# Kernel tuning notes

Measured on AMD Instinct MI355X. Metric: run time of the kernel, lower is better.

The kernel has to match this reference:

```python
import jax, jax.numpy as jnp
import numpy as np

D = 128        # node_state_dim
F = 10         # len(CHOSEN_CONNECTION_FEATURES)
N_IP = 20000
N_CONN = 100000
E = 200000
T = 3


def _seg_mean(vals, ids, n):
    s = jax.ops.segment_sum(vals, ids, num_segments=n)
    c = jax.ops.segment_sum(jnp.ones((vals.shape[0], 1), vals.dtype), ids, num_segments=n)
    return s / jnp.maximum(c, 1.0)


def _gru(x, h, kernel, rec_kernel, bias):
    # keras GRUCell, reset_after=True, gate order [z, r, hh]
    xm = x @ kernel + bias[0]
    hm = h @ rec_kernel + bias[1]
    xz, xr, xh = jnp.split(xm, 3, axis=-1)
    hz, hr, hh = jnp.split(hm, 3, axis=-1)
    z = jax.nn.sigmoid(xz + hz)
    r = jax.nn.sigmoid(xr + hr)
    hcand = jnp.tanh(xh + r * hh)
    return z * h + (1.0 - z) * hcand


def setup_inputs() -> dict:
    key = jax.random.key(0)
    ks = jax.random.split(key, 24)
    s = 0.02
    inp = {
        "feature_connection": jax.random.normal(ks[0], (N_CONN, F), jnp.float32),
        "src_ip_to_connection": jax.random.randint(ks[1], (E,), 0, N_IP, jnp.int32),
        "dst_ip_to_connection": jax.random.randint(ks[2], (E,), 0, N_CONN, jnp.int32),
        "src_connection_to_ip": jax.random.randint(ks[3], (E,), 0, N_CONN, jnp.int32),
        "dst_connection_to_ip": jax.random.randint(ks[4], (E,), 0, N_IP, jnp.int32),
        # message MLPs
        "W_m1": jax.random.normal(ks[5], (2 * D, D), jnp.float32) * s,
        "b_m1": jnp.zeros((D,), jnp.float32),
        "W_m2": jax.random.normal(ks[6], (2 * D, D), jnp.float32) * s,
        "b_m2": jnp.zeros((D,), jnp.float32),
        # GRU cells
        "gru_ip_k": jax.random.normal(ks[7], (D, 3 * D), jnp.float32) * s,
        "gru_ip_r": jax.random.normal(ks[8], (D, 3 * D), jnp.float32) * s,
        "gru_ip_b": jnp.zeros((2, 3 * D), jnp.float32),
        "gru_c_k": jax.random.normal(ks[9], (D, 3 * D), jnp.float32) * s,
        "gru_c_r": jax.random.normal(ks[10], (D, 3 * D), jnp.float32) * s,
        "gru_c_b": jnp.zeros((2, 3 * D), jnp.float32),
        # readout MLP
        "W_r1": jax.random.normal(ks[11], (D, 128), jnp.float32) * s,
        "b_r1": jnp.zeros((128,), jnp.float32),
        "W_r2": jax.random.normal(ks[12], (128, 64), jnp.float32) * s,
        "b_r2": jnp.zeros((64,), jnp.float32),
        "W_r3": jax.random.normal(ks[13], (64, 15), jnp.float32) * s,
        "b_r3": jnp.zeros((15,), jnp.float32),
    }
    return inp


def reference(feature_connection, src_ip_to_connection, dst_ip_to_connection,
              src_connection_to_ip, dst_connection_to_ip,
              W_m1, b_m1, W_m2, b_m2,
              gru_ip_k, gru_ip_r, gru_ip_b,
              gru_c_k, gru_c_r, gru_c_b,
              W_r1, b_r1, W_r2, b_r2, W_r3, b_r3):
    ip_state = jnp.ones((N_IP, D), jnp.float32)
    connection_state = jnp.concatenate(
        [feature_connection, jnp.zeros((N_CONN, D - F), jnp.float32)], axis=1)

    for _ in range(T):
        # ip -> connection messages
        nn_in = jnp.concatenate([ip_state[src_ip_to_connection],
                                 connection_state[dst_ip_to_connection]], axis=1)
        ip_message = jax.nn.relu(nn_in @ W_m1 + b_m1)            # [E, D]
        ip_mean = _seg_mean(ip_message, dst_ip_to_connection, N_CONN)
        # connection -> ip messages
        nn_in2 = jnp.concatenate([connection_state[src_connection_to_ip],
                                  ip_state[dst_connection_to_ip]], axis=1)
        conn_message = jax.nn.relu(nn_in2 @ W_m2 + b_m2)         # [E, D]
        conn_mean = _seg_mean(conn_message, dst_connection_to_ip, N_IP)
        # GRU updates
        ip_state = _gru(conn_mean, ip_state, gru_ip_k, gru_ip_r, gru_ip_b)
        connection_state = _gru(ip_mean, connection_state, gru_c_k, gru_c_r, gru_c_b)

    h = jax.nn.relu(connection_state @ W_r1 + b_r1)
    h = jax.nn.relu(h @ W_r2 + b_r2)
    return jax.nn.softmax(h @ W_r3 + b_r3, axis=-1)              # [N_CONN, 15]
```

## Files before the change

kernel.cpp:

```cpp
#include <hip/hip_runtime.h>
#include <math.h>

#define D 128
#define NF 10
#define N_IP 20000
#define N_CONN 100000
#define NE 200000
#define T_ROUNDS 3

typedef unsigned short u16;
using bf16x8 = __attribute__((ext_vector_type(8))) short;
using floatx4 = __attribute__((ext_vector_type(4))) float;

__device__ inline u16 f2bf(float f) {
  union { float f; unsigned u; } v; v.f = f;
  unsigned u = v.u;
  return (u16)((u + 0x7fffu + ((u >> 16) & 1u)) >> 16);
}
__device__ inline float bf2f(u16 h) {
  union { unsigned u; float f; } v; v.u = ((unsigned)h) << 16; return v.f;
}
__device__ __forceinline__ unsigned cvtpk(float lo, float hi) {
  unsigned r;
  asm("v_cvt_pk_bf16_f32 %0, %1, %2" : "=v"(r) : "v"(lo), "v"(hi));
  return r;
}

__device__ inline float fsigmoid(float s) { return 1.f / (1.f + __expf(-s)); }
__device__ inline float ftanh(float a) {
  a = fminf(fmaxf(a, -15.f), 15.f);
  float e = __expf(2.f * a);
  return (e - 1.f) / (e + 1.f);
}

__device__ __forceinline__ void gld16(const u16* g, u16* l) {
  __builtin_amdgcn_global_load_lds(
      (const __attribute__((address_space(1))) unsigned int*)g,
      (__attribute__((address_space(3))) unsigned int*)l, 16, 0, 0);
}

__global__ void k_setup(u16* __restrict__ ip_state, u16* __restrict__ conn_state,
                        const float* __restrict__ feat, int* __restrict__ cnt,
                        const float* __restrict__ gik, const float* __restrict__ gir,
                        const float* __restrict__ gck, const float* __restrict__ gcr,
                        const float* __restrict__ Wm1, const float* __restrict__ Wm2,
                        const float* __restrict__ Wr1, const float* __restrict__ Wr2,
                        u16* __restrict__ gikb, u16* __restrict__ girb,
                        u16* __restrict__ gckb, u16* __restrict__ gcrb,
                        u16* __restrict__ wm1b, u16* __restrict__ wm2b,
                        u16* __restrict__ wm1t, u16* __restrict__ wm2t,
                        u16* __restrict__ wr1b, u16* __restrict__ wr2b,
                        float* __restrict__ csum, int* __restrict__ gctr) {
  int i = blockIdx.x * blockDim.x + threadIdx.x;
  const int nip = N_IP * D;
  const int nstate = (N_IP + N_CONN) * D;
  if (i < nip) {
    ip_state[i] = 0x3F80;
  } else if (i < nstate) {
    int j = i - nip;
    int r = j >> 7, c = j & 127;
    conn_state[j] = (c < NF) ? f2bf(feat[r * NF + c]) : (u16)0;
  }
  if (i < N_CONN + N_IP) cnt[i] = 0;
  if (i < 2) gctr[i] = 0;
  if (i < 196608) {
    int m = i / 49152, r = i % 49152;
    const float* W = (m == 0) ? gik : (m == 1) ? gir : (m == 2) ? gck : gcr;
    u16* Wb = (m == 0) ? gikb : (m == 1) ? girb : (m == 2) ? gckb : gcrb;
    int col = r >> 7, k = r & 127;
    Wb[r] = f2bf(W[k * 384 + col]);
  } else if (i < 278528) {
    int j = i - 196608;
    int m = j / 16384, r = j % 16384;
    const float* W; u16* Wb; int k0;
    if (m == 0) { W = Wm1; Wb = wm1b; k0 = 128; }
    else if (m == 1) { W = Wm2; Wb = wm2b; k0 = 128; }
    else if (m == 2) { W = Wm1; Wb = wm1t; k0 = 0; }
    else if (m == 3) { W = Wm2; Wb = wm2t; k0 = 0; }
    else { W = Wr1; Wb = wr1b; k0 = 0; }
    int col = r >> 7, k = r & 127;
    Wb[r] = f2bf(W[(k0 + k) * 128 + col]);
  } else if (i < 286720) {
    int r = i - 278528;
    int col = r >> 7, k = r & 127;
    wr2b[r] = f2bf(Wr2[k * 64 + col]);
  } else if (i < 286848) {
    int c = i - 286720;
    float s = 0.f;
    for (int k = 0; k < 128; k++) s += Wm1[k * 128 + c];
    csum[c] = s;
  }
}

__global__ void k_initP_count(const float* __restrict__ csum, const float* __restrict__ feat,
                              const float* __restrict__ Wm2,
                              u16* __restrict__ P1, u16* __restrict__ P2,
                              const int* __restrict__ d1, const int* __restrict__ d2,
                              int* __restrict__ c1, int* __restrict__ c2) {
  int i = blockIdx.x * blockDim.x + threadIdx.x;
  if (i < NE) {
    atomicAdd(&c1[d1[i]], 1);
    atomicAdd(&c2[d2[i]], 1);
  }
  const int n1 = N_IP * 16;
  const int n2 = N_CONN * 16;
  if (i < n1) {
    int r = i >> 4, g = i & 15;
    u16 v[8];
#pragma unroll
    for (int k = 0; k < 8; k++) v[k] = f2bf(csum[g * 8 + k]);
    *(uint4*)(P1 + (size_t)r * 128 + g * 8) = *(const uint4*)v;
  } else if (i < n1 + n2) {
    int j = i - n1;
    int r = j >> 4, g = j & 15;
    float acc[8] = {0.f, 0.f, 0.f, 0.f, 0.f, 0.f, 0.f, 0.f};
#pragma unroll
    for (int k = 0; k < NF; k++) {
      float f = feat[(size_t)r * NF + k];
      const float* wrow = Wm2 + (size_t)k * 128 + g * 8;
#pragma unroll
      for (int c = 0; c < 8; c++) acc[c] += f * wrow[c];
    }
    u16 v[8];
#pragma unroll
    for (int c = 0; c < 8; c++) v[c] = f2bf(acc[c]);
    *(uint4*)(P2 + (size_t)r * 128 + g * 8) = *(const uint4*)v;
  }
}

__global__ void k_alloc(const int* __restrict__ cnt1, int* __restrict__ off1,
                        int* __restrict__ cur1, int n1, int nb1,
                        const int* __restrict__ cnt2, int* __restrict__ off2,
                        int* __restrict__ cur2, int n2, int* __restrict__ gctr) {
  const int* cnt; int* off; int* cur; int n, b; int* g;
  if ((int)blockIdx.x < nb1) {
    cnt = cnt1; off = off1; cur = cur1; n = n1; b = blockIdx.x; g = gctr;
  } else {
    cnt = cnt2; off = off2; cur = cur2; n = n2; b = blockIdx.x - nb1; g = gctr + 1;
  }
  int t = threadIdx.x;
  int base = b * 1024 + t * 4;
  int vals[4]; int s = 0;
#pragma unroll
  for (int i = 0; i < 4; i++) {
    int j = base + i;
    vals[i] = (j < n) ? cnt[j] : 0;
    s += vals[i];
  }
  int lane = t & 63, wv = t >> 6;
  int x = s;
  for (int d = 1; d < 64; d <<= 1) { int y = __shfl_up(x, d, 64); if (lane >= d) x += y; }
  __shared__ int wsum[4];
  __shared__ int gbase;
  if (lane == 63) wsum[wv] = x;
  __syncthreads();
  int add = 0;
  for (int i = 0; i < wv; i++) add += wsum[i];
  if (t == 0) gbase = atomicAdd(g, wsum[0] + wsum[1] + wsum[2] + wsum[3]);
  __syncthreads();
  int run = gbase + add + x - s;
#pragma unroll
  for (int i = 0; i < 4; i++) {
    int j = base + i;
    if (j < n) { off[j] = run; cur[j] = run; }
    run += vals[i];
  }
}

__global__ void k_scatter(const int* __restrict__ s1, const int* __restrict__ d1,
                          const int* __restrict__ s2, const int* __restrict__ d2,
                          int* __restrict__ cur1, int* __restrict__ cur2,
                          int* __restrict__ o1, int* __restrict__ o2) {
  int e = blockIdx.x * blockDim.x + threadIdx.x;
  if (e >= NE) return;
  int p1 = atomicAdd(&cur1[d1[e]], 1);
  o1[p1] = s1[e];
  int p2 = atomicAdd(&cur2[d2[e]], 1);
  o2[p2] = s2[e];
}

__global__ __launch_bounds__(512, 4) void k_msggru(
    u16* __restrict__ st1, const u16* __restrict__ wq1, const float* __restrict__ qb1,
    const u16* __restrict__ P1g, const int* __restrict__ srcs1g,
    const int* __restrict__ off1g, const int* __restrict__ cnt1g,
    const u16* __restrict__ wx1, const u16* __restrict__ wh1, const float* __restrict__ gb1,
    const u16* __restrict__ wp1, u16* __restrict__ Pn1, int r1, int tiles1,
    u16* __restrict__ st2, const u16* __restrict__ wq2, const float* __restrict__ qb2,
    const u16* __restrict__ P2g, const int* __restrict__ srcs2g,
    const int* __restrict__ off2g, const int* __restrict__ cnt2g,
    const u16* __restrict__ wx2, const u16* __restrict__ wh2, const float* __restrict__ gb2,
    const u16* __restrict__ wp2, u16* __restrict__ Pn2, int r2, int doP,
    const u16* __restrict__ w1r, const float* __restrict__ b1r,
    const u16* __restrict__ w2r, const float* __restrict__ b2r,
    const float* __restrict__ W3r, const float* __restrict__ b3r,
    float* __restrict__ outp, int doRd) {
  __shared__ __align__(16) char smem[65536];
  u16* Wls = (u16*)smem;
  u16* Qb = (u16*)smem;
  u16* bufA = (u16*)smem;
  u16* bufB = (u16*)(smem + 12288);
  u16* Hls = (u16*)(smem + 32768);
  u16* H; const u16* Wqb; const float* qbias; const u16* P;
  const int* srcs; const int* off; const int* cnt;
  const u16* Wxb; const u16* Whb; const float* gbias;
  const u16* Wpt; u16* Pn; int rows, bm;
  const bool side2 = (int)blockIdx.x >= tiles1;
  if (!side2) {
    H = st1; Wqb = wq1; qbias = qb1; P = P1g; srcs = srcs1g; off = off1g; cnt = cnt1g;
    Wxb = wx1; Whb = wh1; gbias = gb1; Wpt = wp1; Pn = Pn1; rows = r1; bm = blockIdx.x * 128;
  } else {
    H = st2; Wqb = wq2; qbias = qb2; P = P2g; srcs = srcs2g; off = off2g; cnt = cnt2g;
    Wxb = wx2; Whb = wh2; gbias = gb2; Wpt = wp2; Pn = Pn2; rows = r2;
    bm = (blockIdx.x - tiles1) * 128;
  }
  const int tid = threadIdx.x, wv = tid >> 6, lane = tid & 63;
  const int lrow = lane & 15, quad = lane >> 4;
#pragma unroll
  for (int j = 0; j < 4; j++) {
    int c = j * 512 + tid;
    int row = c >> 4, sl = c & 15;
    gld16(Wqb + (size_t)row * 128 + ((sl ^ (row & 15)) * 8), Wls + (size_t)c * 8);
  }
#pragma unroll
  for (int i = 0; i < 4; i++) {
    int c = i * 512 + tid;
    int row = c >> 4, sl = c & 15;
    gld16(H + (size_t)(bm + row) * 128 + ((sl ^ (row & 15)) * 8), Hls + (size_t)c * 8);
  }
  int oArr[4], nArr[4];
#pragma unroll
  for (int it = 0; it < 4; it++) {
    int nl = (it * 512 + tid) >> 4;
    int node = bm + nl;
    oArr[it] = (node < rows) ? off[node] : 0;
    nArr[it] = (node < rows) ? cnt[node] : 0;
  }
  __syncthreads();
  bf16x8 ah[4];
#pragma unroll
  for (int ks = 0; ks < 4; ks++)
    ah[ks] = *(const bf16x8*)(Hls + (size_t)(wv * 16 + lrow) * 128 + (((ks * 4 + quad) ^ lrow) * 8));
  floatx4 acc[8];
#pragma unroll
  for (int ct = 0; ct < 8; ct++) acc[ct] = {0.f, 0.f, 0.f, 0.f};
#pragma unroll
  for (int ks = 0; ks < 4; ks++) {
#pragma unroll
    for (int ct = 0; ct < 8; ct++) {
      bf16x8 b = *(const bf16x8*)(Wls + (size_t)(ct * 16 + lrow) * 128 + (((4 * ks + quad) ^ lrow) * 8));
      acc[ct] = __builtin_amdgcn_mfma_f32_16x16x32_bf16(ah[ks], b, acc[ct], 0, 0, 0);
    }
  }
  __syncthreads();
  {
    const int lr = wv * 16 + quad * 4;
#pragma unroll
    for (int ct = 0; ct < 8; ct++) {
      int col = ct * 16 + lrow;
      float bv = qbias[col];
      unsigned p01 = cvtpk(acc[ct][0] + bv, acc[ct][1] + bv);
      unsigned p23 = cvtpk(acc[ct][2] + bv, acc[ct][3] + bv);
      Qb[(size_t)(lr + 0) * 128 + col] = (u16)p01;
      Qb[(size_t)(lr + 1) * 128 + col] = (u16)(p01 >> 16);
      Qb[(size_t)(lr + 2) * 128 + col] = (u16)p23;
      Qb[(size_t)(lr + 3) * 128 + col] = (u16)(p23 >> 16);
    }
  }
  __syncthreads();
#pragma unroll
  for (int it = 0; it < 4; it++) {
    int task = it * 512 + tid;
    int nl = task >> 4, g = task & 15;
    int node = bm + nl;
    if (node >= rows) continue;
    int c8 = g << 3;
    float q[8];
    {
      uint4 qv = *(const uint4*)(Qb + (size_t)nl * 128 + c8);
      unsigned qq[4] = {qv.x, qv.y, qv.z, qv.w};
#pragma unroll
      for (int k = 0; k < 4; k++) {
        q[2 * k] = __uint_as_float(qq[k] << 16);
        q[2 * k + 1] = __uint_as_float(qq[k] & 0xffff0000u);
      }
    }
    float acg[8] = {0.f, 0.f, 0.f, 0.f, 0.f, 0.f, 0.f, 0.f};
    int o = oArr[it], n = nArr[it];
    for (int i = 0; i < n; i += 4) {
      int rem = n - i;
      int s0 = srcs[o + i];
      int s1 = srcs[o + i + (rem > 1 ? 1 : 0)];
      int s2 = srcs[o + i + (rem > 2 ? 2 : 0)];
      int s3 = srcs[o + i + (rem > 3 ? 3 : 0)];
      uint4 v0 = *(const uint4*)(P + (size_t)s0 * 128 + c8);
      uint4 v1 = *(const uint4*)(P + (size_t)s1 * 128 + c8);
      uint4 v2 = *(const uint4*)(P + (size_t)s2 * 128 + c8);
// ... 96 lines not shown
    int gel = lrow & 7;
    float hn[4];
#pragma unroll
    for (int reg = 0; reg < 4; reg++) {
      int lr = lr0 + reg;
      float xz = gacc[0][0][reg] + bxz;
      float xr = gacc[1][0][reg] + bxr;
      float xh = gacc[2][0][reg] + bxh;
      float hz = gacc[0][1][reg] + bhz;
      float hr = gacc[1][1][reg] + bhr;
      float hh = gacc[2][1][reg] + bhh;
      float z = fsigmoid(xz + hz);
      float rr = fsigmoid(xr + hr);
      float hc = ftanh(xh + rr * hh);
      const u16* hp = Hls + (size_t)lr * 128 + ((ggr ^ (lr & 15)) * 8) + gel;
      float hold = bf2f(*hp);
      hn[reg] = z * hold + (1.f - z) * hc;
    }
    unsigned q01 = cvtpk(hn[0], hn[1]);
    unsigned q23 = cvtpk(hn[2], hn[3]);
#define HPTR(R) (Hls + (size_t)(lr0 + (R)) * 128 + ((ggr ^ ((lr0 + (R)) & 15)) * 8) + gel)
    *HPTR(0) = (u16)q01;
    *HPTR(1) = (u16)(q01 >> 16);
    *HPTR(2) = (u16)q23;
    *HPTR(3) = (u16)(q23 >> 16);
#undef HPTR
  }
  __syncthreads();
#pragma unroll
  for (int i = 0; i < 4; i++) {
    int c = i * 512 + tid;
    int row = c >> 4, g = c & 15;
    int grow = bm + row;
    if (grow < rows)
      *(uint4*)(H + (size_t)grow * 128 + g * 8) =
          *(const uint4*)(Hls + (size_t)row * 128 + ((g ^ (row & 15)) * 8));
  }
  if (doP) {
    bf16x8 ah2[4];
#pragma unroll
    for (int ks = 0; ks < 4; ks++)
      ah2[ks] = *(const bf16x8*)(Hls + (size_t)(wv * 16 + lrow) * 128 + (((ks * 4 + quad) ^ lrow) * 8));
#pragma unroll
    for (int j = 0; j < 4; j++) {
      int c = j * 512 + tid;
      int row = c >> 4, sl = c & 15;
      gld16(Wpt + (size_t)row * 128 + ((sl ^ (row & 15)) * 8), Wls + (size_t)c * 8);
    }
    __syncthreads();
#pragma unroll
    for (int ct = 0; ct < 8; ct++) acc[ct] = {0.f, 0.f, 0.f, 0.f};
#pragma unroll
    for (int ks = 0; ks < 4; ks++) {
#pragma unroll
      for (int ct = 0; ct < 8; ct++) {
        bf16x8 b = *(const bf16x8*)(Wls + (size_t)(ct * 16 + lrow) * 128 + (((4 * ks + quad) ^ lrow) * 8));
        acc[ct] = __builtin_amdgcn_mfma_f32_16x16x32_bf16(ah2[ks], b, acc[ct], 0, 0, 0);
      }
    }
    u16* Cls = Hls;
    {
      const int lr = wv * 16 + quad * 4;
#pragma unroll
      for (int ct = 0; ct < 8; ct++) {
        int col = ct * 16 + lrow;
        unsigned p01 = cvtpk(acc[ct][0], acc[ct][1]);
        unsigned p23 = cvtpk(acc[ct][2], acc[ct][3]);
        Cls[(size_t)(lr + 0) * 128 + col] = (u16)p01;
        Cls[(size_t)(lr + 1) * 128 + col] = (u16)(p01 >> 16);
        Cls[(size_t)(lr + 2) * 128 + col] = (u16)p23;
        Cls[(size_t)(lr + 3) * 128 + col] = (u16)(p23 >> 16);
      }
    }
    __syncthreads();
#pragma unroll
    for (int i = 0; i < 4; i++) {
      int c = i * 512 + tid;
      int row = c >> 4, g = c & 15;
      int grow = bm + row;
      if (grow < rows)
        *(uint4*)(Pn + (size_t)grow * 128 + g * 8) =
            *(const uint4*)(Cls + (size_t)row * 128 + g * 8);
    }
    return;
  }
  if (!doRd || !side2) return;
  bf16x8 ar[4];
#pragma unroll
  for (int ks = 0; ks < 4; ks++)
    ar[ks] = *(const bf16x8*)(Hls + (size_t)(wv * 16 + lrow) * 128 + (((ks * 4 + quad) ^ lrow) * 8));
#pragma unroll
  for (int j = 0; j < 4; j++) {
    int c = j * 512 + tid;
    int row = c >> 4, sl = c & 15;
    gld16(w1r + (size_t)row * 128 + ((sl ^ (row & 15)) * 8), Wls + (size_t)c * 8);
  }
  __syncthreads();
#pragma unroll
  for (int ct = 0; ct < 8; ct++) acc[ct] = {0.f, 0.f, 0.f, 0.f};
#pragma unroll
  for (int ks = 0; ks < 4; ks++) {
#pragma unroll
    for (int ct = 0; ct < 8; ct++) {
      bf16x8 b = *(const bf16x8*)(Wls + (size_t)(ct * 16 + lrow) * 128 + (((4 * ks + quad) ^ lrow) * 8));
      acc[ct] = __builtin_amdgcn_mfma_f32_16x16x32_bf16(ar[ks], b, acc[ct], 0, 0, 0);
    }
  }
#pragma unroll
  for (int ct = 0; ct < 8; ct++) {
    int col = ct * 16 + lrow;
    float bv = b1r[col];
    int ggr = 2 * ct + (lrow >> 3);
    int gel = lrow & 7;
    unsigned p01 = cvtpk(fmaxf(acc[ct][0] + bv, 0.f), fmaxf(acc[ct][1] + bv, 0.f));
    unsigned p23 = cvtpk(fmaxf(acc[ct][2] + bv, 0.f), fmaxf(acc[ct][3] + bv, 0.f));
#define H1PTR(R) (Hls + (size_t)(lr0 + (R)) * 128 + ((ggr ^ ((lr0 + (R)) & 15)) * 8) + gel)
    *H1PTR(0) = (u16)p01;
    *H1PTR(1) = (u16)(p01 >> 16);
    *H1PTR(2) = (u16)p23;
    *H1PTR(3) = (u16)(p23 >> 16);
#undef H1PTR
  }
  __syncthreads();
#pragma unroll
  for (int j = 0; j < 2; j++) {
    int c = j * 512 + tid;
    int row = c >> 4, sl = c & 15;
    gld16(w2r + (size_t)row * 128 + ((sl ^ (row & 15)) * 8), Wls + (size_t)c * 8);
  }
  __syncthreads();
  bf16x8 a2[4];
#pragma unroll
  for (int ks = 0; ks < 4; ks++)
    a2[ks] = *(const bf16x8*)(Hls + (size_t)(wv * 16 + lrow) * 128 + (((ks * 4 + quad) ^ lrow) * 8));
  floatx4 acc2[4];
#pragma unroll
  for (int ct = 0; ct < 4; ct++) acc2[ct] = {0.f, 0.f, 0.f, 0.f};
#pragma unroll
  for (int ks = 0; ks < 4; ks++) {
#pragma unroll
    for (int ct = 0; ct < 4; ct++) {
      bf16x8 b = *(const bf16x8*)(Wls + (size_t)(ct * 16 + lrow) * 128 + (((4 * ks + quad) ^ lrow) * 8));
      acc2[ct] = __builtin_amdgcn_mfma_f32_16x16x32_bf16(a2[ks], b, acc2[ct], 0, 0, 0);
    }
  }
  __syncthreads();
  u16* H2 = (u16*)smem;
  float* W3ls = (float*)(smem + 18432);
  float* b3ls = (float*)(smem + 18432 + 3840);
#pragma unroll
  for (int ct = 0; ct < 4; ct++) {
    int col = ct * 16 + lrow;
    float bv = b2r[col];
#pragma unroll
    for (int reg = 0; reg < 4; reg++)
      H2[(size_t)(lr0 + reg) * 72 + col] = f2bf(fmaxf(acc2[ct][reg] + bv, 0.f));
  }
  for (int l = tid; l < 960; l += 512) W3ls[l] = W3r[l];
  if (tid < 15) b3ls[tid] = b3r[tid];
  __syncthreads();
  {
    int col = tid & 15;
    int rb = (tid >> 4) * 4;
    float lg[4] = {0.f, 0.f, 0.f, 0.f};
    if (col < 15) {
      float b3v = b3ls[col];
      lg[0] = b3v; lg[1] = b3v; lg[2] = b3v; lg[3] = b3v;
      for (int k8 = 0; k8 < 64; k8 += 8) {
        float w[8];
#pragma unroll
        for (int j = 0; j < 8; j++) w[j] = W3ls[(k8 + j) * 15 + col];
#pragma unroll
        for (int r = 0; r < 4; r++) {
          bf16x8 hv = *(const bf16x8*)(H2 + (size_t)(rb + r) * 72 + k8);
#pragma unroll
          for (int j = 0; j < 8; j++) lg[r] += bf2f((u16)hv[j]) * w[j];
        }
      }
    }
#pragma unroll
    for (int r = 0; r < 4; r++) {
      float v = (col < 15) ? lg[r] : -3.0e38f;
      float m = v;
#pragma unroll
      for (int d = 1; d < 16; d <<= 1) m = fmaxf(m, __shfl_xor(m, d, 16));
      float e = (col < 15) ? __expf(lg[r] - m) : 0.f;
      float s = e;
#pragma unroll
      for (int d = 1; d < 16; d <<= 1) s += __shfl_xor(s, d, 16);
      int gr2 = bm + rb + r;
      if (col < 15 && gr2 < rows) outp[(size_t)gr2 * 15 + col] = e / s;
    }
  }
}

extern "C" void kernel_launch(void* const* d_in, const int* in_sizes, int n_in,
                              void* d_out, int out_size, void* d_ws, size_t ws_size,
                              hipStream_t stream) {
  const float* feat = (const float*)d_in[0];
  const int* src1 = (const int*)d_in[1];
  const int* dst1 = (const int*)d_in[2];
  const int* src2 = (const int*)d_in[3];
  const int* dst2 = (const int*)d_in[4];
  const float* Wm1 = (const float*)d_in[5];
  const float* bm1 = (const float*)d_in[6];
  const float* Wm2 = (const float*)d_in[7];
  const float* bm2 = (const float*)d_in[8];
  const float* gik = (const float*)d_in[9];
  const float* gir = (const float*)d_in[10];
  const float* gib = (const float*)d_in[11];
  const float* gck = (const float*)d_in[12];
  const float* gcr = (const float*)d_in[13];
  const float* gcb = (const float*)d_in[14];
  const float* Wr1 = (const float*)d_in[15];
  const float* br1 = (const float*)d_in[16];
  const float* Wr2 = (const float*)d_in[17];
  const float* br2 = (const float*)d_in[18];
  const float* Wr3 = (const float*)d_in[19];
  const float* br3 = (const float*)d_in[20];
  float* out = (float*)d_out;

  u16* w16 = (u16*)d_ws;
  size_t o = 0;
  u16* ip_state = w16 + o;   o += (size_t)N_IP * D;
  u16* conn_state = w16 + o; o += (size_t)N_CONN * D;
  u16* P1a = w16 + o;        o += (size_t)N_IP * D;
  u16* P2a = w16 + o;        o += (size_t)N_CONN * D;
  u16* P1b = w16 + o;        o += (size_t)N_IP * D;
  u16* P2b = w16 + o;        o += (size_t)N_CONN * D;
  u16* gikb = w16 + o;       o += 49152;
  u16* girb = w16 + o;       o += 49152;
  u16* gckb = w16 + o;       o += 49152;
  u16* gcrb = w16 + o;       o += 49152;
  u16* wm1b = w16 + o;       o += 16384;
  u16* wm2b = w16 + o;       o += 16384;
  u16* wm1t = w16 + o;       o += 16384;
  u16* wm2t = w16 + o;       o += 16384;
  u16* wr1b = w16 + o;       o += 16384;
  u16* wr2b = w16 + o;       o += 8192;
  float* csum = (float*)(w16 + o); o += 256;
  int* ip = (int*)(w16 + o);
  int* cnt1 = ip;  ip += N_CONN;
  int* cnt2 = ip;  ip += N_IP;
  int* off1 = ip;  ip += N_CONN;
  int* off2 = ip;  ip += N_IP;
  int* cur1 = ip;  ip += N_CONN;
  int* cur2 = ip;  ip += N_IP;
  int* srcs1 = ip; ip += NE;
  int* srcs2 = ip; ip += NE;
  int* gctr = ip;  ip += 8;

  const int BT = 256;

  const int nstate = (N_IP + N_CONN) * D;
  k_setup<<<(nstate + BT - 1) / BT, BT, 0, stream>>>(
      ip_state, conn_state, feat, cnt1,
      gik, gir, gck, gcr, Wm1, Wm2, Wr1, Wr2,
      gikb, girb, gckb, gcrb, wm1b, wm2b, wm1t, wm2t, wr1b, wr2b, csum, gctr);
  const int nPinit = (N_IP + N_CONN) * 16;
  k_initP_count<<<(nPinit + BT - 1) / BT, BT, 0, stream>>>(
      csum, feat, Wm2, P1a, P2a, dst1, dst2, cnt1, cnt2);

  const int nb1 = (N_CONN + 1023) / 1024, nb2 = (N_IP + 1023) / 1024;
  k_alloc<<<nb1 + nb2, 256, 0, stream>>>(cnt1, off1, cur1, N_CONN, nb1,
                                         cnt2, off2, cur2, N_IP, gctr);
  k_scatter<<<(NE + BT - 1) / BT, BT, 0, stream>>>(src1, dst1, src2, dst2,
                                                   cur1, cur2, srcs1, srcs2);

  const int t128ip = (N_IP + 127) / 128;
  const int t128cn = (N_CONN + 127) / 128;

  u16* P1buf[2] = {P1a, P1b};
  u16* P2buf[2] = {P2a, P2b};
  for (int t = 0; t < T_ROUNDS; t++) {
    int cu = t & 1, nx = cu ^ 1;
    int last = (t == T_ROUNDS - 1);
    k_msggru<<<t128ip + t128cn, 512, 0, stream>>>(
        ip_state, wm2b, bm2, P2buf[cu], srcs2, off2, cnt2, gikb, girb, gib,
        wm1t, P1buf[nx], N_IP, t128ip,
        conn_state, wm1b, bm1, P1buf[cu], srcs1, off1, cnt1, gckb, gcrb, gcb,
        wm2t, P2buf[nx], N_CONN, last ? 0 : 1,
        wr1b, br1, wr2b, br2, Wr3, br3, out, last ? 1 : 0);
  }
}
```

Baseline: 435.3 us.

## Fuse prep and round kernels into persistent cooperative launches with grid sync

Replaces the chain of setup, count, alloc, scatter and per-round message/GRU launches with two cooperative kernels that loop over work and use grid-wide barriers between phases. The aim is to remove per-launch overhead and idle gaps between the seven dependent kernels. The round kernel runs a fixed grid of 512 blocks that stride over tiles, which may cut parallelism or leave load imbalance compared with one block per tile. A fallback to the original separate launches is kept for when a cooperative launch fails.

```diff
diff --git a/kernel.cpp b/kernel.cpp
--- a/kernel.cpp
+++ b/kernel.cpp
@@ -1,5 +1,8 @@
 #include <hip/hip_runtime.h>
+#include <hip/hip_cooperative_groups.h>
 #include <math.h>
+
+namespace cg = cooperative_groups;
 
 #define D 128
 #define NF 10
@@ -8,6 +11,13 @@
 #define NE 200000
 #define T_ROUNDS 3
 
+#define NSTATE ((N_IP + N_CONN) * D)
+#define NPI ((N_IP + N_CONN) * 16)
+#define NB1 ((N_CONN + 1023) / 1024)
+#define NB2 ((N_IP + 1023) / 1024)
+#define T128IP ((N_IP + 127) / 128)
+#define T128CN ((N_CONN + 127) / 128)
+
 typedef unsigned short u16;
 using bf16x8 = __attribute__((ext_vector_type(8))) short;
 using floatx4 = __attribute__((ext_vector_type(4))) float;
@@ -39,105 +49,94 @@
       (__attribute__((address_space(3))) unsigned int*)l, 16, 0, 0);
 }
 
-__global__ void k_setup(u16* __restrict__ ip_state, u16* __restrict__ conn_state,
-                        const float* __restrict__ feat, int* __restrict__ cnt,
-                        const float* __restrict__ gik, const float* __restrict__ gir,
-                        const float* __restrict__ gck, const float* __restrict__ gcr,
-                        const float* __restrict__ Wm1, const float* __restrict__ Wm2,
-                        const float* __restrict__ Wr1, const float* __restrict__ Wr2,
-                        u16* __restrict__ gikb, u16* __restrict__ girb,
-                        u16* __restrict__ gckb, u16* __restrict__ gcrb,
-                        u16* __restrict__ wm1b, u16* __restrict__ wm2b,
-                        u16* __restrict__ wm1t, u16* __restrict__ wm2t,
-                        u16* __restrict__ wr1b, u16* __restrict__ wr2b,
-                        float* __restrict__ csum, int* __restrict__ gctr) {
-  int i = blockIdx.x * blockDim.x + threadIdx.x;
+struct GArgs {
+  const float* feat; const int* src1; const int* dst1; const int* src2; const int* dst2;
+  const float* Wm1; const float* bm1; const float* Wm2; const float* bm2;
+  const float* gik; const float* gir; const float* gib;
+  const float* gck; const float* gcr; const float* gcb;
+  const float* Wr1; const float* br1; const float* Wr2; const float* br2;
+  const float* Wr3; const float* br3;
+  float* out;
+  u16 *ip_state, *conn_state, *P1a, *P2a, *P1b, *P2b;
+  u16 *gikb, *girb, *gckb, *gcrb, *wm1b, *wm2b, *wm1t, *wm2t, *wr1b, *wr2b;
+  float* csum;
+  int *cnt1, *cnt2, *off1, *off2, *cur1, *cur2, *srcs1, *srcs2, *gctr;
+};
+
+__device__ __forceinline__ void setup_body(const GArgs& a, int i) {
   const int nip = N_IP * D;
-  const int nstate = (N_IP + N_CONN) * D;
   if (i < nip) {
-    ip_state[i] = 0x3F80;
-  } else if (i < nstate) {
+    a.ip_state[i] = 0x3F80;
+  } else {
     int j = i - nip;
     int r = j >> 7, c = j & 127;
-    conn_state[j] = (c < NF) ? f2bf(feat[r * NF + c]) : (u16)0;
-  }
-  if (i < N_CONN + N_IP) cnt[i] = 0;
-  if (i < 2) gctr[i] = 0;
+    a.conn_state[j] = (c < NF) ? f2bf(a.feat[r * NF + c]) : (u16)0;
+  }
+  if (i < N_CONN + N_IP) a.cnt1[i] = 0;
+  if (i < 2) a.gctr[i] = 0;
   if (i < 196608) {
     int m = i / 49152, r = i % 49152;
-    const float* W = (m == 0) ? gik : (m == 1) ? gir : (m == 2) ? gck : gcr;
-    u16* Wb = (m == 0) ? gikb : (m == 1) ? girb : (m == 2) ? gckb : gcrb;
+    const float* W = (m == 0) ? a.gik : (m == 1) ? a.gir : (m == 2) ? a.gck : a.gcr;
+    u16* Wb = (m == 0) ? a.gikb : (m == 1) ? a.girb : (m == 2) ? a.gckb : a.gcrb;
     int col = r >> 7, k = r & 127;
     Wb[r] = f2bf(W[k * 384 + col]);
   } else if (i < 278528) {
     int j = i - 196608;
     int m = j / 16384, r = j % 16384;
     const float* W; u16* Wb; int k0;
-    if (m == 0) { W = Wm1; Wb = wm1b; k0 = 128; }
-    else if (m == 1) { W = Wm2; Wb = wm2b; k0 = 128; }
-    else if (m == 2) { W = Wm1; Wb = wm1t; k0 = 0; }
-    else if (m == 3) { W = Wm2; Wb = wm2t; k0 = 0; }
-    else { W = Wr1; Wb = wr1b; k0 = 0; }
+    if (m == 0) { W = a.Wm1; Wb = a.wm1b; k0 = 128; }
+    else if (m == 1) { W = a.Wm2; Wb = a.wm2b; k0 = 128; }
+    else if (m == 2) { W = a.Wm1; Wb = a.wm1t; k0 = 0; }
+    else if (m == 3) { W = a.Wm2; Wb = a.wm2t; k0 = 0; }
+    else { W = a.Wr1; Wb = a.wr1b; k0 = 0; }
     int col = r >> 7, k = r & 127;
     Wb[r] = f2bf(W[(k0 + k) * 128 + col]);
   } else if (i < 286720) {
     int r = i - 278528;
     int col = r >> 7, k = r & 127;
-    wr2b[r] = f2bf(Wr2[k * 64 + col]);
+    a.wr2b[r] = f2bf(a.Wr2[k * 64 + col]);
   } else if (i < 286848) {
     int c = i - 286720;
     float s = 0.f;
-    for (int k = 0; k < 128; k++) s += Wm1[k * 128 + c];
-    csum[c] = s;
-  }
-}
-
-__global__ void k_initP_count(const float* __restrict__ csum, const float* __restrict__ feat,
-                              const float* __restrict__ Wm2,
-                              u16* __restrict__ P1, u16* __restrict__ P2,
-                              const int* __restrict__ d1, const int* __restrict__ d2,
-                              int* __restrict__ c1, int* __restrict__ c2) {
-  int i = blockIdx.x * blockDim.x + threadIdx.x;
+    for (int k = 0; k < 128; k++) s += a.Wm1[k * 128 + c];
+    a.csum[c] = s;
+  }
+}
+
+__device__ __forceinline__ void initp_body(const GArgs& a, int i) {
   if (i < NE) {
-    atomicAdd(&c1[d1[i]], 1);
-    atomicAdd(&c2[d2[i]], 1);
+    atomicAdd(&a.cnt1[a.dst1[i]], 1);
+    atomicAdd(&a.cnt2[a.dst2[i]], 1);
   }
   const int n1 = N_IP * 16;
-  const int n2 = N_CONN * 16;
   if (i < n1) {
     int r = i >> 4, g = i & 15;
     u16 v[8];
 #pragma unroll
-    for (int k = 0; k < 8; k++) v[k] = f2bf(csum[g * 8 + k]);
-    *(uint4*)(P1 + (size_t)r * 128 + g * 8) = *(const uint4*)v;
-  } else if (i < n1 + n2) {
+    for (int k = 0; k < 8; k++) v[k] = f2bf(a.csum[g * 8 + k]);
+    *(uint4*)(a.P1a + (size_t)r * 128 + g * 8) = *(const uint4*)v;
+  } else {
     int j = i - n1;
     int r = j >> 4, g = j & 15;
     float acc[8] = {0.f, 0.f, 0.f, 0.f, 0.f, 0.f, 0.f, 0.f};
 #pragma unroll
     for (int k = 0; k < NF; k++) {
-      float f = feat[(size_t)r * NF + k];
-      const float* wrow = Wm2 + (size_t)k * 128 + g * 8;
+      float f = a.feat[(size_t)r * NF + k];
+      const float* wrow = a.Wm2 + (size_t)k * 128 + g * 8;
 #pragma unroll
       for (int c = 0; c < 8; c++) acc[c] += f * wrow[c];
     }
     u16 v[8];
 #pragma unroll
     for (int c = 0; c < 8; c++) v[c] = f2bf(acc[c]);
-    *(uint4*)(P2 + (size_t)r * 128 + g * 8) = *(const uint4*)v;
-  }
-}
-
-__global__ void k_alloc(const int* __restrict__ cnt1, int* __restrict__ off1,
-                        int* __restrict__ cur1, int n1, int nb1,
-                        const int* __restrict__ cnt2, int* __restrict__ off2,
-                        int* __restrict__ cur2, int n2, int* __restrict__ gctr) {
+    *(uint4*)(a.P2a + (size_t)r * 128 + g * 8) = *(const uint4*)v;
+  }
+}
+
+__device__ void alloc_chunk(const GArgs& a, int bc) {
   const int* cnt; int* off; int* cur; int n, b; int* g;
-  if ((int)blockIdx.x < nb1) {
-    cnt = cnt1; off = off1; cur = cur1; n = n1; b = blockIdx.x; g = gctr;
-  } else {
-    cnt = cnt2; off = off2; cur = cur2; n = n2; b = blockIdx.x - nb1; g = gctr + 1;
-  }
+  if (bc < NB1) { cnt = a.cnt1; off = a.off1; cur = a.cur1; n = N_CONN; b = bc; g = a.gctr; }
+  else { cnt = a.cnt2; off = a.off2; cur = a.cur2; n = N_IP; b = bc - NB1; g = a.gctr + 1; }
   int t = threadIdx.x;
   int base = b * 1024 + t * 4;
   int vals[4]; int s = 0;
@@ -167,33 +166,15 @@
   }
 }
 
-__global__ void k_scatter(const int* __restrict__ s1, const int* __restrict__ d1,
-                          const int* __restrict__ s2, const int* __restrict__ d2,
-                          int* __restrict__ cur1, int* __restrict__ cur2,
-                          int* __restrict__ o1, int* __restrict__ o2) {
-  int e = blockIdx.x * blockDim.x + threadIdx.x;
-  if (e >= NE) return;
-  int p1 = atomicAdd(&cur1[d1[e]], 1);
-  o1[p1] = s1[e];
-  int p2 = atomicAdd(&cur2[d2[e]], 1);
-  o2[p2] = s2[e];
-}
-
-__global__ __launch_bounds__(512, 4) void k_msggru(
-    u16* __restrict__ st1, const u16* __restrict__ wq1, const float* __restrict__ qb1,
-    const u16* __restrict__ P1g, const int* __restrict__ srcs1g,
-    const int* __restrict__ off1g, const int* __restrict__ cnt1g,
-    const u16* __restrict__ wx1, const u16* __restrict__ wh1, const float* __restrict__ gb1,
-    const u16* __restrict__ wp1, u16* __restrict__ Pn1, int r1, int tiles1,
-    u16* __restrict__ st2, const u16* __restrict__ wq2, const float* __restrict__ qb2,
-    const u16* __restrict__ P2g, const int* __restrict__ srcs2g,
-    const int* __restrict__ off2g, const int* __restrict__ cnt2g,
-    const u16* __restrict__ wx2, const u16* __restrict__ wh2, const float* __restrict__ gb2,
-    const u16* __restrict__ wp2, u16* __restrict__ Pn2, int r2, int doP,
-    const u16* __restrict__ w1r, const float* __restrict__ b1r,
-    const u16* __restrict__ w2r, const float* __restrict__ b2r,
-    const float* __restrict__ W3r, const float* __restrict__ b3r,
-    float* __restrict__ outp, int doRd) {
+__device__ __forceinline__ void scatter_body(const GArgs& a, int e) {
+  int p1 = atomicAdd(&a.cur1[a.dst1[e]], 1);
+  a.srcs1[p1] = a.src1[e];
+  int p2 = atomicAdd(&a.cur2[a.dst2[e]], 1);
+  a.srcs2[p2] = a.src2[e];
+}
+
+__device__ void tile_body(const GArgs& a, int vb, int tiles1, int doP, int doRd,
+                          const u16* P1r, const u16* P2r, u16* P1w, u16* P2w) {
   __shared__ __align__(16) char smem[65536];
   u16* Wls = (u16*)smem;
   u16* Qb = (u16*)smem;
@@ -203,15 +184,15 @@
   u16* H; const u16* Wqb; const float* qbias; const u16* P;
   const int* srcs; const int* off; const int* cnt;
   const u16* Wxb; const u16* Whb; const float* gbias;
-  const u16* Wpt; u16* Pn; int rows, bm;
-  const bool side2 = (int)blockIdx.x >= tiles1;
-  if (!side2) {
-    H = st1; Wqb = wq1; qbias = qb1; P = P1g; srcs = srcs1g; off = off1g; cnt = cnt1g;
-    Wxb = wx1; Whb = wh1; gbias = gb1; Wpt = wp1; Pn = Pn1; rows = r1; bm = blockIdx.x * 128;
+  const u16* Wpt; u16* Pn; int rows, bm; bool side2;
+  if (vb < tiles1) {
+    H = a.ip_state; Wqb = a.wm2b; qbias = a.bm2; P = P2r; srcs = a.srcs2;
+    off = a.off2; cnt = a.cnt2; Wxb = a.gikb; Whb = a.girb; gbias = a.gib;
+    Wpt = a.wm1t; Pn = P1w; rows = N_IP; bm = vb * 128; side2 = false;
   } else {
-    H = st2; Wqb = wq2; qbias = qb2; P = P2g; srcs = srcs2g; off = off2g; cnt = cnt2g;
-    Wxb = wx2; Whb = wh2; gbias = gb2; Wpt = wp2; Pn = Pn2; rows = r2;
-    bm = (blockIdx.x - tiles1) * 128;
+    H = a.conn_state; Wqb = a.wm1b; qbias = a.bm1; P = P1r; srcs = a.srcs1;
+    off = a.off1; cnt = a.cnt1; Wxb = a.gckb; Whb = a.gcrb; gbias = a.gcb;
+    Wpt = a.wm2t; Pn = P2w; rows = N_CONN; bm = (vb - tiles1) * 128; side2 = true;
   }
   const int tid = threadIdx.x, wv = tid >> 6, lane = tid & 63;
   const int lrow = lane & 15, quad = lane >> 4;
@@ -474,204 +455,235 @@
         *(uint4*)(Pn + (size_t)grow * 128 + g * 8) =
             *(const uint4*)(Cls + (size_t)row * 128 + g * 8);
     }
-    return;
-  }
-  if (!doRd || !side2) return;
-  bf16x8 ar[4];
-#pragma unroll
-  for (int ks = 0; ks < 4; ks++)
-    ar[ks] = *(const bf16x8*)(Hls + (size_t)(wv * 16 + lrow) * 128 + (((ks * 4 + quad) ^ lrow) * 8));
-#pragma unroll
-  for (int j = 0; j < 4; j++) {
-    int c = j * 512 + tid;
-    int row = c >> 4, sl = c & 15;
-    gld16(w1r + (size_t)row * 128 + ((sl ^ (row & 15)) * 8), Wls + (size_t)c * 8);
-  }
-  __syncthreads();
-#pragma unroll
-  for (int ct = 0; ct < 8; ct++) acc[ct] = {0.f, 0.f, 0.f, 0.f};
-#pragma unroll
-  for (int ks = 0; ks < 4; ks++) {
+  } else if (doRd && side2) {
+    bf16x8 ar[4];
+#pragma unroll
+    for (int ks = 0; ks < 4; ks++)
+      ar[ks] = *(const bf16x8*)(Hls + (size_t)(wv * 16 + lrow) * 128 + (((ks * 4 + quad) ^ lrow) * 8));
+#pragma unroll
+    for (int j = 0; j < 4; j++) {
+      int c = j * 512 + tid;
+      int row = c >> 4, sl = c & 15;
+      gld16(a.wr1b + (size_t)row * 128 + ((sl ^ (row & 15)) * 8), Wls + (size_t)c * 8);
+    }
+    __syncthreads();
+#pragma unroll
+    for (int ct = 0; ct < 8; ct++) acc[ct] = {0.f, 0.f, 0.f, 0.f};
+#pragma unroll
+    for (int ks = 0; ks < 4; ks++) {
+#pragma unroll
+      for (int ct = 0; ct < 8; ct++) {
+        bf16x8 b = *(const bf16x8*)(Wls + (size_t)(ct * 16 + lrow) * 128 + (((4 * ks + quad) ^ lrow) * 8));
+        acc[ct] = __builtin_amdgcn_mfma_f32_16x16x32_bf16(ar[ks], b, acc[ct], 0, 0, 0);
+      }
+    }
 #pragma unroll
     for (int ct = 0; ct < 8; ct++) {
-      bf16x8 b = *(const bf16x8*)(Wls + (size_t)(ct * 16 + lrow) * 128 + (((4 * ks + quad) ^ lrow) * 8));
-      acc[ct] = __builtin_amdgcn_mfma_f32_16x16x32_bf16(ar[ks], b, acc[ct], 0, 0, 0);
-    }
-  }
-#pragma unroll
-  for (int ct = 0; ct < 8; ct++) {
-    int col = ct * 16 + lrow;
-    float bv = b1r[col];
-    int ggr = 2 * ct + (lrow >> 3);
-    int gel = lrow & 7;
-    unsigned p01 = cvtpk(fmaxf(acc[ct][0] + bv, 0.f), fmaxf(acc[ct][1] + bv, 0.f));
-    unsigned p23 = cvtpk(fmaxf(acc[ct][2] + bv, 0.f), fmaxf(acc[ct][3] + bv, 0.f));
+      int col = ct * 16 + lrow;
+      float bv = a.br1[col];
+      int ggr = 2 * ct + (lrow >> 3);
+      int gel = lrow & 7;
+      unsigned p01 = cvtpk(fmaxf(acc[ct][0] + bv, 0.f), fmaxf(acc[ct][1] + bv, 0.f));
+      unsigned p23 = cvtpk(fmaxf(acc[ct][2] + bv, 0.f), fmaxf(acc[ct][3] + bv, 0.f));
 #define H1PTR(R) (Hls + (size_t)(lr0 + (R)) * 128 + ((ggr ^ ((lr0 + (R)) & 15)) * 8) + gel)
-    *H1PTR(0) = (u16)p01;
-    *H1PTR(1) = (u16)(p01 >> 16);
-    *H1PTR(2) = (u16)p23;
-    *H1PTR(3) = (u16)(p23 >> 16);
+      *H1PTR(0) = (u16)p01;
+      *H1PTR(1) = (u16)(p01 >> 16);
+      *H1PTR(2) = (u16)p23;
+      *H1PTR(3) = (u16)(p23 >> 16);
 #undef H1PTR
-  }
-  __syncthreads();
-#pragma unroll
-  for (int j = 0; j < 2; j++) {
-    int c = j * 512 + tid;
-    int row = c >> 4, sl = c & 15;
-    gld16(w2r + (size_t)row * 128 + ((sl ^ (row & 15)) * 8), Wls + (size_t)c * 8);
-  }
-  __syncthreads();
-  bf16x8 a2[4];
-#pragma unroll
-  for (int ks = 0; ks < 4; ks++)
-    a2[ks] = *(const bf16x8*)(Hls + (size_t)(wv * 16 + lrow) * 128 + (((ks * 4 + quad) ^ lrow) * 8));
-  floatx4 acc2[4];
-#pragma unroll
-  for (int ct = 0; ct < 4; ct++) acc2[ct] = {0.f, 0.f, 0.f, 0.f};
-#pragma unroll
-  for (int ks = 0; ks < 4; ks++) {
+    }
+    __syncthreads();
+#pragma unroll
+    for (int j = 0; j < 2; j++) {
+      int c = j * 512 + tid;
+      int row = c >> 4, sl = c & 15;
+      gld16(a.wr2b + (size_t)row * 128 + ((sl ^ (row & 15)) * 8), Wls + (size_t)c * 8);
+    }
+    __syncthreads();
+    bf16x8 a2[4];
+#pragma unroll
+    for (int ks = 0; ks < 4; ks++)
+      a2[ks] = *(const bf16x8*)(Hls + (size_t)(wv * 16 + lrow) * 128 + (((ks * 4 + quad) ^ lrow) * 8));
+    floatx4 acc2[4];
+#pragma unroll
+    for (int ct = 0; ct < 4; ct++) acc2[ct] = {0.f, 0.f, 0.f, 0.f};
+#pragma unroll
+    for (int ks = 0; ks < 4; ks++) {
+#pragma unroll
+      for (int ct = 0; ct < 4; ct++) {
+        bf16x8 b = *(const bf16x8*)(Wls + (size_t)(ct * 16 + lrow) * 128 + (((4 * ks + quad) ^ lrow) * 8));
+        acc2[ct] = __builtin_amdgcn_mfma_f32_16x16x32_bf16(a2[ks], b, acc2[ct], 0, 0, 0);
+      }
+    }
+    __syncthreads();
+    u16* H2 = (u16*)smem;
+    float* W3ls = (float*)(smem + 18432);
+    float* b3ls = (float*)(smem + 18432 + 3840);
 #pragma unroll
     for (int ct = 0; ct < 4; ct++) {
-      bf16x8 b = *(const bf16x8*)(Wls + (size_t)(ct * 16 + lrow) * 128 + (((4 * ks + quad) ^ lrow) * 8));
-      acc2[ct] = __builtin_amdgcn_mfma_f32_16x16x32_bf16(a2[ks], b, acc2[ct], 0, 0, 0);
-    }
-  }
-  __syncthreads();
-  u16* H2 = (u16*)smem;
-  float* W3ls = (float*)(smem + 18432);
-  float* b3ls = (float*)(smem + 18432 + 3840);
-#pragma unroll
-  for (int ct = 0; ct < 4; ct++) {
-    int col = ct * 16 + lrow;
-    float bv = b2r[col];
-#pragma unroll
-    for (int reg = 0; reg < 4; reg++)
-      H2[(size_t)(lr0 + reg) * 72 + col] = f2bf(fmaxf(acc2[ct][reg] + bv, 0.f));
-  }
-  for (int l = tid; l < 960; l += 512) W3ls[l] = W3r[l];
-  if (tid < 15) b3ls[tid] = b3r[tid];
-  __syncthreads();
-  {
-    int col = tid & 15;
-    int rb = (tid >> 4) * 4;
-    float lg[4] = {0.f, 0.f, 0.f, 0.f};
-    if (col < 15) {
-      float b3v = b3ls[col];
-      lg[0] = b3v; lg[1] = b3v; lg[2] = b3v; lg[3] = b3v;
-      for (int k8 = 0; k8 < 64; k8 += 8) {
-        float w[8];
-#pragma unroll
-        for (int j = 0; j < 8; j++) w[j] = W3ls[(k8 + j) * 15 + col];
-#pragma unroll
-        for (int r = 0; r < 4; r++) {
-          bf16x8 hv = *(const bf16x8*)(H2 + (size_t)(rb + r) * 72 + k8);
-#pragma unroll
-          for (int j = 0; j < 8; j++) lg[r] += bf2f((u16)hv[j]) * w[j];
+      int col = ct * 16 + lrow;
+      float bv = a.br2[col];
+#pragma unroll
+      for (int reg = 0; reg < 4; reg++)
+        H2[(size_t)(lr0 + reg) * 72 + col] = f2bf(fmaxf(acc2[ct][reg] + bv, 0.f));
+    }
+    for (int l = tid; l < 960; l += 512) W3ls[l] = a.Wr3[l];
+    if (tid < 15) b3ls[tid] = a.br3[tid];
+    __syncthreads();
+    {
+      int col = tid & 15;
+      int rb = (tid >> 4) * 4;
+      float lg[4] = {0.f, 0.f, 0.f, 0.f};
+      if (col < 15) {
+        float b3v = b3ls[col];
+        lg[0] = b3v; lg[1] = b3v; lg[2] = b3v; lg[3] = b3v;
+        for (int k8 = 0; k8 < 64; k8 += 8) {
+          float w[8];
+#pragma unroll
+          for (int j = 0; j < 8; j++) w[j] = W3ls[(k8 + j) * 15 + col];
+#pragma unroll
+          for (int r = 0; r < 4; r++) {
+            bf16x8 hv = *(const bf16x8*)(H2 + (size_t)(rb + r) * 72 + k8);
+#pragma unroll
+            for (int j = 0; j < 8; j++) lg[r] += bf2f((u16)hv[j]) * w[j];
+          }
         }
       }
-    }
-#pragma unroll
-    for (int r = 0; r < 4; r++) {
-      float v = (col < 15) ? lg[r] : -3.0e38f;
-      float m = v;
-#pragma unroll
-      for (int d = 1; d < 16; d <<= 1) m = fmaxf(m, __shfl_xor(m, d, 16));
-      float e = (col < 15) ? __expf(lg[r] - m) : 0.f;
-      float s = e;
-#pragma unroll
-      for (int d = 1; d < 16; d <<= 1) s += __shfl_xor(s, d, 16);
-      int gr2 = bm + rb + r;
-      if (col < 15 && gr2 < rows) outp[(size_t)gr2 * 15 + col] = e / s;
-    }
-  }
+#pragma unroll
+      for (int r = 0; r < 4; r++) {
+        float v = (col < 15) ? lg[r] : -3.0e38f;
+        float m = v;
+#pragma unroll
+        for (int d = 1; d < 16; d <<= 1) m = fmaxf(m, __shfl_xor(m, d, 16));
+        float e = (col < 15) ? __expf(lg[r] - m) : 0.f;
+        float s = e;
+#pragma unroll
+        for (int d = 1; d < 16; d <<= 1) s += __shfl_xor(s, d, 16);
+        int gr2 = bm + rb + r;
+        if (col < 15 && gr2 < rows) a.out[(size_t)gr2 * 15 + col] = e / s;
+      }
+    }
+  }
+  __syncthreads();
+}
+
+__global__ __launch_bounds__(256) void k_prep(GArgs a) {
+  cg::grid_group g = cg::this_grid();
+  const int gsz = gridDim.x * blockDim.x;
+  const int gtid = blockIdx.x * blockDim.x + threadIdx.x;
+  for (int i = gtid; i < NSTATE; i += gsz) setup_body(a, i);
+  g.sync();
+  for (int i = gtid; i < NPI; i += gsz) initp_body(a, i);
+  g.sync();
+  if ((int)blockIdx.x < NB1 + NB2) alloc_chunk(a, blockIdx.x);
+  g.sync();
+  for (int e = gtid; e < NE; e += gsz) scatter_body(a, e);
+}
+
+__global__ __launch_bounds__(512, 4) void k_rounds(GArgs a) {
+  cg::grid_group g = cg::this_grid();
+  const int ntile = T128IP + T128CN;
+  for (int t = 0; t < T_ROUNDS; t++) {
+    const int cu = t & 1, nx = cu ^ 1;
+    const int last = (t == T_ROUNDS - 1);
+    const u16* P1r = cu ? a.P1b : a.P1a; const u16* P2r = cu ? a.P2b : a.P2a;
+    u16* P1w = nx ? a.P1b : a.P1a;       u16* P2w = nx ? a.P2b : a.P2a;
+    for (int vb = blockIdx.x; vb < ntile; vb += gridDim.x)
+      tile_body(a, vb, T128IP, last ? 0 : 1, last ? 1 : 0, P1r, P2r, P1w, P2w);
+    if (!last) g.sync();
+  }
+}
+
+__global__ void k_setup_fb(GArgs a) {
+  int i = blockIdx.x * blockDim.x + threadIdx.x;
+  if (i < NSTATE) setup_body(a, i);
+}
+__global__ void k_initp_fb(GArgs a) {
+  int i = blockIdx.x * blockDim.x + threadIdx.x;
+  if (i < NPI) initp_body(a, i);
+}
+__global__ void k_alloc_fb(GArgs a) { alloc_chunk(a, blockIdx.x); }
+__global__ void k_scatter_fb(GArgs a) {
+  int e = blockIdx.x * blockDim.x + threadIdx.x;
+  if (e < NE) scatter_body(a, e);
+}
+__global__ __launch_bounds__(512, 4) void k_msggru_fb(GArgs a, int t) {
+  const int cu = t & 1, nx = cu ^ 1;
+  const int last = (t == T_ROUNDS - 1);
+  const u16* P1r = cu ? a.P1b : a.P1a; const u16* P2r = cu ? a.P2b : a.P2a;
+  u16* P1w = nx ? a.P1b : a.P1a;       u16* P2w = nx ? a.P2b : a.P2a;
+  tile_body(a, blockIdx.x, T128IP, last ? 0 : 1, last ? 1 : 0, P1r, P2r, P1w, P2w);
 }
 
 extern "C" void kernel_launch(void* const* d_in, const int* in_sizes, int n_in,
                               void* d_out, int out_size, void* d_ws, size_t ws_size,
                               hipStream_t stream) {
-  const float* feat = (const float*)d_in[0];
-  const int* src1 = (const int*)d_in[1];
-  const int* dst1 = (const int*)d_in[2];
-  const int* src2 = (const int*)d_in[3];
-  const int* dst2 = (const int*)d_in[4];
-  const float* Wm1 = (const float*)d_in[5];
-  const float* bm1 = (const float*)d_in[6];
-  const float* Wm2 = (const float*)d_in[7];
-  const float* bm2 = (const float*)d_in[8];
-  const float* gik = (const float*)d_in[9];
-  const float* gir = (const float*)d_in[10];
-  const float* gib = (const float*)d_in[11];
-  const float* gck = (const float*)d_in[12];
-  const float* gcr = (const float*)d_in[13];
-  const float* gcb = (const float*)d_in[14];
-  const float* Wr1 = (const float*)d_in[15];
-  const float* br1 = (const float*)d_in[16];
-  const float* Wr2 = (const float*)d_in[17];
-  const float* br2 = (const float*)d_in[18];
-  const float* Wr3 = (const float*)d_in[19];
-  const float* br3 = (const float*)d_in[20];
-  float* out = (float*)d_out;
+  GArgs a;
+  a.feat = (const float*)d_in[0];
+  a.src1 = (const int*)d_in[1];
+  a.dst1 = (const int*)d_in[2];
+  a.src2 = (const int*)d_in[3];
+  a.dst2 = (const int*)d_in[4];
+  a.Wm1 = (const float*)d_in[5];
+  a.bm1 = (const float*)d_in[6];
+  a.Wm2 = (const float*)d_in[7];
+  a.bm2 = (const float*)d_in[8];
+  a.gik = (const float*)d_in[9];
+  a.gir = (const float*)d_in[10];
+  a.gib = (const float*)d_in[11];
+  a.gck = (const float*)d_in[12];
+  a.gcr = (const float*)d_in[13];
+  a.gcb = (const float*)d_in[14];
+  a.Wr1 = (const float*)d_in[15];
+  a.br1 = (const float*)d_in[16];
+  a.Wr2 = (const float*)d_in[17];
+  a.br2 = (const float*)d_in[18];
+  a.Wr3 = (const float*)d_in[19];
+  a.br3 = (const float*)d_in[20];
+  a.out = (float*)d_out;
 
   u16* w16 = (u16*)d_ws;
   size_t o = 0;
-  u16* ip_state = w16 + o;   o += (size_t)N_IP * D;
-  u16* conn_state = w16 + o; o += (size_t)N_CONN * D;
-  u16* P1a = w16 + o;        o += (size_t)N_IP * D;
-  u16* P2a = w16 + o;        o += (size_t)N_CONN * D;
-  u16* P1b = w16 + o;        o += (size_t)N_IP * D;
-  u16* P2b = w16 + o;        o += (size_t)N_CONN * D;
-  u16* gikb = w16 + o;       o += 49152;
-  u16* girb = w16 + o;       o += 49152;
-  u16* gckb = w16 + o;       o += 49152;
-  u16* gcrb = w16 + o;       o += 49152;
-  u16* wm1b = w16 + o;       o += 16384;
-  u16* wm2b = w16 + o;       o += 16384;
-  u16* wm1t = w16 + o;       o += 16384;
-  u16* wm2t = w16 + o;       o += 16384;
-  u16* wr1b = w16 + o;       o += 16384;
-  u16* wr2b = w16 + o;       o += 8192;
-  float* csum = (float*)(w16 + o); o += 256;
+  a.ip_state = w16 + o;   o += (size_t)N_IP * D;
+  a.conn_state = w16 + o; o += (size_t)N_CONN * D;
+  a.P1a = w16 + o;        o += (size_t)N_IP * D;
+  a.P2a = w16 + o;        o += (size_t)N_CONN * D;
+  a.P1b = w16 + o;        o += (size_t)N_IP * D;
+  a.P2b = w16 + o;        o += (size_t)N_CONN * D;
+  a.gikb = w16 + o;       o += 49152;
+  a.girb = w16 + o;       o += 49152;
+  a.gckb = w16 + o;       o += 49152;
+  a.gcrb = w16 + o;       o += 49152;
+  a.wm1b = w16 + o;       o += 16384;
+  a.wm2b = w16 + o;       o += 16384;
+  a.wm1t = w16 + o;       o += 16384;
+  a.wm2t = w16 + o;       o += 16384;
+  a.wr1b = w16 + o;       o += 16384;
+  a.wr2b = w16 + o;       o += 8192;
+  a.csum = (float*)(w16 + o); o += 256;
   int* ip = (int*)(w16 + o);
-  int* cnt1 = ip;  ip += N_CONN;
-  int* cnt2 = ip;  ip += N_IP;
-  int* off1 = ip;  ip += N_CONN;
-  int* off2 = ip;  ip += N_IP;
-  int* cur1 = ip;  ip += N_CONN;
-  int* cur2 = ip;  ip += N_IP;
-  int* srcs1 = ip; ip += NE;
-  int* srcs2 = ip; ip += NE;
-  int* gctr = ip;  ip += 8;
-
-  const int BT = 256;
-
-  const int nstate = (N_IP + N_CONN) * D;
-  k_setup<<<(nstate + BT - 1) / BT, BT, 0, stream>>>(
-      ip_state, conn_state, feat, cnt1,
-      gik, gir, gck, gcr, Wm1, Wm2, Wr1, Wr2,
-      gikb, girb, gckb, gcrb, wm1b, wm2b, wm1t, wm2t, wr1b, wr2b, csum, gctr);
-  const int nPinit = (N_IP + N_CONN) * 16;
-  k_initP_count<<<(nPinit + BT - 1) / BT, BT, 0, stream>>>(
-      csum, feat, Wm2, P1a, P2a, dst1, dst2, cnt1, cnt2);
-
-  const int nb1 = (N_CONN + 1023) / 1024, nb2 = (N_IP + 1023) / 1024;
-  k_alloc<<<nb1 + nb2, 256, 0, stream>>>(cnt1, off1, cur1, N_CONN, nb1,
-                                         cnt2, off2, cur2, N_IP, gctr);
-  k_scatter<<<(NE + BT - 1) / BT, BT, 0, stream>>>(src1, dst1, src2, dst2,
-                                                   cur1, cur2, srcs1, srcs2);
-
-  const int t128ip = (N_IP + 127) / 128;
-  const int t128cn = (N_CONN + 127) / 128;
-
-  u16* P1buf[2] = {P1a, P1b};
-  u16* P2buf[2] = {P2a, P2b};
-  for (int t = 0; t < T_ROUNDS; t++) {
-    int cu = t & 1, nx = cu ^ 1;
-    int last = (t == T_ROUNDS - 1);
-    k_msggru<<<t128ip + t128cn, 512, 0, stream>>>(
-        ip_state, wm2b, bm2, P2buf[cu], srcs2, off2, cnt2, gikb, girb, gib,
-        wm1t, P1buf[nx], N_IP, t128ip,
-        conn_state, wm1b, bm1, P1buf[cu], srcs1, off1, cnt1, gckb, gcrb, gcb,
-        wm2t, P2buf[nx], N_CONN, last ? 0 : 1,
-        wr1b, br1, wr2b, br2, Wr3, br3, out, last ? 1 : 0);
-  }
-}
+  a.cnt1 = ip;  ip += N_CONN;
+  a.cnt2 = ip;  ip += N_IP;
+  a.off1 = ip;  ip += N_CONN;
+  a.off2 = ip;  ip += N_IP;
+  a.cur1 = ip;  ip += N_CONN;
+  a.cur2 = ip;  ip += N_IP;
+  a.srcs1 = ip; ip += NE;
+  a.srcs2 = ip; ip += NE;
+  a.gctr = ip;  ip += 8;
+
+  void* kp[1] = {(void*)&a};
+  hipError_t err = hipLaunchCooperativeKernel(k_prep, dim3(1024), dim3(256), kp, 0, stream);
+  if (err == hipSuccess)
+    err = hipLaunchCooperativeKernel(k_rounds, dim3(512), dim3(512), kp, 0, stream);
+  if (err != hipSuccess) {
+    (void)hipGetLastError();
+    const int BT = 256;
+    k_setup_fb<<<(NSTATE + BT - 1) / BT, BT, 0, stream>>>(a);
+    k_initp_fb<<<(NPI + BT - 1) / BT, BT, 0, stream>>>(a);
+    k_alloc_fb<<<NB1 + NB2, 256, 0, stream>>>(a);
+    k_scatter_fb<<<(NE + BT - 1) / BT, BT, 0, stream>>>(a);
+    for (int t = 0; t < T_ROUNDS; t++)
+      k_msggru_fb<<<T128IP + T128CN, 512, 0, stream>>>(a, t);
+  }
+}
```

Result: slower. 1.103 ms (+153.4%).
